# Kernel tuning notes

Hardware: AMD Instinct MI355X
Metric: run time of the kernel (lower is better)

## Reference

```python
import jax, jax.numpy as jnp
import numpy as np

B, S = 2, 2048          # batch, seq_len (tokens flattened to T=B*S)
HID = 2048              # hidden_size
H = 16                  # num_heads
DN, DR, DV = 128, 64, 128   # qk_nope_head_dim, qk_rope_head_dim, v_head_dim
QKD = DN + DR           # qk_head_dim = 192
QLR, KVR = 1536, 512    # q_lora_rank, kv_lora_rank
THETA = 10000.0
EPS = 1e-6
SCALE = QKD ** -0.5


def rmsnorm(x, w):
    return x * jax.lax.rsqrt(jnp.mean(x * x, axis=-1, keepdims=True) + EPS) * w


def rope_gptj(x, pos):
    # non-neox (interleaved / GPT-J) style on partial head dim DR
    # x: [T, Hx, DR], pos: [T]
    half = DR // 2
    inv_freq = 1.0 / (THETA ** (jnp.arange(half, dtype=jnp.float32) * 2.0 / DR))
    ang = pos.astype(jnp.float32)[:, None] * inv_freq[None, :]      # [T, half]
    cos = jnp.cos(ang)[:, None, :]
    sin = jnp.sin(ang)[:, None, :]
    x1 = x[..., 0::2]
    x2 = x[..., 1::2]
    o1 = x1 * cos - x2 * sin
    o2 = x2 * cos + x1 * sin
    return jnp.stack([o1, o2], axis=-1).reshape(x.shape)


def setup_inputs() -> dict:
    key = jax.random.key(0)
    ks = jax.random.split(key, 8)
    T = B * S
    positions = jnp.tile(jnp.arange(S, dtype=jnp.int64 if jax.config.jax_enable_x64 else jnp.int32), B)
    hidden_states = jax.random.normal(ks[0], (T, HID), dtype=jnp.float32)
    s = 0.02
    Wqa = jax.random.normal(ks[1], (HID, QLR), dtype=jnp.float32) * s
    q_a_ln_w = jnp.ones((QLR,), dtype=jnp.float32)
    Wqb = jax.random.normal(ks[2], (QLR, H * QKD), dtype=jnp.float32) * s
    Wkva = jax.random.normal(ks[3], (HID, KVR + DR), dtype=jnp.float32) * s
    kv_a_ln_w = jnp.ones((KVR,), dtype=jnp.float32)
    Wkvb = jax.random.normal(ks[4], (KVR, H * (DN + DV)), dtype=jnp.float32) * s
    Wo = jax.random.normal(ks[5], (H * DV, HID), dtype=jnp.float32) * s
    return {"positions": positions, "hidden_states": hidden_states, "Wqa": Wqa,
            "q_a_ln_w": q_a_ln_w, "Wqb": Wqb, "Wkva": Wkva,
            "kv_a_ln_w": kv_a_ln_w, "Wkvb": Wkvb, "Wo": Wo}


def reference(positions, hidden_states, Wqa, q_a_ln_w, Wqb, Wkva, kv_a_ln_w, Wkvb, Wo):
    T = hidden_states.shape[0]
    # --- Q path: low-rank compression ---
    ckq = hidden_states @ Wqa                       # [T, QLR]
    q_c = rmsnorm(ckq, q_a_ln_w)
    q = (q_c @ Wqb).reshape(T, H, QKD)              # [T, H, 192]
    q_nope, q_pe = q[..., :DN], q[..., DN:]
    # --- KV path: latent compression + shared rope key ---
    kv_no_split = hidden_states @ Wkva              # [T, KVR+DR]
    kv_c, k_pe = kv_no_split[:, :KVR], kv_no_split[:, KVR:]
    kv_c_normed = rmsnorm(kv_c, kv_a_ln_w)
    kv = (kv_c_normed @ Wkvb).reshape(T, H, DN + DV)
    k_nope, v = kv[..., :DN], kv[..., DN:]
    # --- RoPE on partial dims (non-neox) ---
    q_pe = rope_gptj(q_pe, positions)               # [T, H, DR]
    k_pe = rope_gptj(k_pe[:, None, :], positions)   # [T, 1, DR]
    # --- assemble full q/k per batch ---
    qf = jnp.concatenate([q_nope, q_pe], axis=-1).reshape(B, S, H, QKD)
    kf = jnp.concatenate([k_nope, jnp.broadcast_to(k_pe, (T, H, DR))], axis=-1).reshape(B, S, H, QKD)
    vf = v.reshape(B, S, H, DV)
    # --- causal attention ---
    scores = jnp.einsum('bqhd,bkhd->bhqk', qf, kf) * SCALE
    mask = jnp.tril(jnp.ones((S, S), dtype=bool))
    scores = jnp.where(mask[None, None], scores, jnp.finfo(scores.dtype).min)
    probs = jax.nn.softmax(scores, axis=-1)
    attn = jnp.einsum('bhqk,bkhd->bqhd', probs, vf).reshape(T, H * DV)
    # --- output projection ---
    return attn @ Wo                                # [T, HID]
```

## Files before the change

### kernel.cpp

```cpp
#include <hip/hip_runtime.h>
#include <hip/hip_bf16.h>

typedef __hip_bfloat16 bf16;
typedef short bf16x8 __attribute__((ext_vector_type(8)));
typedef float f32x4 __attribute__((ext_vector_type(4)));

#define MFMA16(a, b, c) __builtin_amdgcn_mfma_f32_16x16x32_bf16((a), (b), (c), 0, 0, 0)

__device__ __forceinline__ short f2bs(float f) {
  bf16 h = __float2bfloat16(f);
  return __builtin_bit_cast(short, h);
}
__device__ __forceinline__ float bs2f(short s) {
  return __bfloat162float(__builtin_bit_cast(bf16, s));
}

__device__ __forceinline__ void gload16(const void* g, const void* l) {
  __builtin_amdgcn_global_load_lds(
      (const __attribute__((address_space(1))) unsigned int*)g,
      (__attribute__((address_space(3))) unsigned int*)l, 16, 0, 0);
}

__global__ __launch_bounds__(256) void cvt3(
    const float* __restrict__ s0, bf16* __restrict__ d0, int n0,
    const float* __restrict__ s1, bf16* __restrict__ d1, int n1,
    const float* __restrict__ s2, bf16* __restrict__ d2)
{
  int i = blockIdx.x * 256 + threadIdx.x;
  const float* s; bf16* d; int idx;
  if (i < n0)            { s = s0; d = d0; idx = i; }
  else if (i < n0 + n1)  { s = s1; d = d1; idx = i - n0; }
  else                   { s = s2; d = d2; idx = i - n0 - n1; }
  const float4* sp = (const float4*)s;
  float4 a = sp[2 * idx], b = sp[2 * idx + 1];
  union { uint4 v; short sh[8]; } o;
  o.sh[0] = f2bs(a.x); o.sh[1] = f2bs(a.y); o.sh[2] = f2bs(a.z); o.sh[3] = f2bs(a.w);
  o.sh[4] = f2bs(b.x); o.sh[5] = f2bs(b.y); o.sh[6] = f2bs(b.z); o.sh[7] = f2bs(b.w);
  ((uint4*)d)[idx] = o.v;
}

__global__ __launch_bounds__(256) void t_cvt(const float* __restrict__ src,
                                             bf16* __restrict__ dst, int K, int N) {
  __shared__ __align__(16) short Ts[64][72];
  const long n0 = (long)blockIdx.x * 64, k0 = (long)blockIdx.y * 64;
  const int r = threadIdx.x >> 2, c4 = threadIdx.x & 3;
  const float* s = src + (k0 + r) * (long)N + n0 + c4 * 16;
  #pragma unroll
  for (int j = 0; j < 4; ++j) {
    float4 v = *(const float4*)(s + j * 4);
    Ts[r][c4 * 16 + j * 4 + 0] = f2bs(v.x);
    Ts[r][c4 * 16 + j * 4 + 1] = f2bs(v.y);
    Ts[r][c4 * 16 + j * 4 + 2] = f2bs(v.z);
    Ts[r][c4 * 16 + j * 4 + 3] = f2bs(v.w);
  }
  __syncthreads();
  union { uint4 v; short sh[8]; } o0, o1;
  #pragma unroll
  for (int j = 0; j < 8; ++j) o0.sh[j] = Ts[c4 * 16 + j][r];
  #pragma unroll
  for (int j = 0; j < 8; ++j) o1.sh[j] = Ts[c4 * 16 + 8 + j][r];
  *(uint4*)(dst + (n0 + r) * (long)K + k0 + c4 * 16)     = o0.v;
  *(uint4*)(dst + (n0 + r) * (long)K + k0 + c4 * 16 + 8) = o1.v;
}

template<bool F32OUT>
__device__ __forceinline__ void gemm_core(
    short* As, short* Bs,
    const bf16* __restrict__ A, const bf16* __restrict__ BT, void* __restrict__ Cv,
    int N, int K, int lda, int ldb, int ldc, bf16* __restrict__ C2, int ncut,
    int nx, int nwg, int lin)
{
  const int tid = threadIdx.x, lane = tid & 63, w = tid >> 6;
  const int l15 = lane & 15, l4 = lane >> 4;
  const int wr = w >> 1, wc = w & 1;
  const int sl = (lin & 7) * (nwg >> 3) + (lin >> 3);
  const long bm = (long)(sl / nx) * 128, bn = (long)(sl % nx) * 128;
  f32x4 acc[4][4] = {};

  const int srow = tid >> 3;
  const int scs = (tid & 7) ^ (srow & 7);
  const int rsw = l15 & 7;

  for (int k0 = 0; k0 < K; k0 += 64) {
    __syncthreads();
    #pragma unroll
    for (int j = 0; j < 4; ++j) {
      const unsigned lb = __builtin_amdgcn_readfirstlane((j * 256 + w * 64) * 16);
      gload16(A + (bm + j * 32 + srow) * (long)lda + k0 + scs * 8, (char*)As + lb);
      gload16(BT + (bn + j * 32 + srow) * (long)ldb + k0 + scs * 8, (char*)Bs + lb);
    }
    __syncthreads();
    #pragma unroll
    for (int kk = 0; kk < 2; ++kk) {
      bf16x8 a[4], b[4];
      const int slot = (kk * 4 + l4) ^ rsw;
      #pragma unroll
      for (int mi = 0; mi < 4; ++mi)
        a[mi] = *(const bf16x8*)&As[(wr * 64 + mi * 16 + l15) * 64 + slot * 8];
      #pragma unroll
      for (int ni = 0; ni < 4; ++ni)
        b[ni] = *(const bf16x8*)&Bs[(wc * 64 + ni * 16 + l15) * 64 + slot * 8];
      #pragma unroll
      for (int mi = 0; mi < 4; ++mi)
        #pragma unroll
        for (int ni = 0; ni < 4; ++ni)
          acc[mi][ni] = MFMA16(a[mi], b[ni], acc[mi][ni]);
    }
  }
  #pragma unroll
  for (int mi = 0; mi < 4; ++mi)
    #pragma unroll
    for (int ni = 0; ni < 4; ++ni)
      #pragma unroll
      for (int r = 0; r < 4; ++r) {
        long row = bm + wr * 64 + mi * 16 + l4 * 4 + r;
        long col = bn + wc * 64 + ni * 16 + l15;
        float v = acc[mi][ni][r];
        if (F32OUT) {
          ((float*)Cv)[row * ldc + col] = v;
        } else if (C2 && col >= ncut) {
          C2[row * 640 + (col - ncut)] = __float2bfloat16(v);
        } else {
          ((bf16*)Cv)[row * (long)ldc + col] = __float2bfloat16(v);
        }
      }
}

template<bool F32OUT>
__global__ __launch_bounds__(256) void gemm_v4(
    const bf16* __restrict__ A, const bf16* __restrict__ BT, void* __restrict__ Cv,
    int N, int K, int lda, int ldb, int ldc, bf16* __restrict__ C2, int ncut)
{
  __shared__ __align__(16) short As[128 * 64];
  __shared__ __align__(16) short Bs[128 * 64];
  const int nx = gridDim.x, nwg = nx * gridDim.y;
  const int lin = blockIdx.y * nx + blockIdx.x;
  gemm_core<F32OUT>(As, Bs, A, BT, Cv, N, K, lda, ldb, ldc, C2, ncut, nx, nwg, lin);
}

__global__ __launch_bounds__(256) void gemm_dual(
    const bf16* __restrict__ A0, const bf16* __restrict__ B0, bf16* __restrict__ C0,
    const bf16* __restrict__ A1, const bf16* __restrict__ B1, bf16* __restrict__ C1)
{
  __shared__ __align__(16) short As[128 * 64];
  __shared__ __align__(16) short Bs[128 * 64];
  const int bid = blockIdx.x;
  if (bid < 768)
    gemm_core<false>(As, Bs, A0, B0, C0, 3072, 1536, 1536, 1536, 3072, nullptr, 0,
                     24, 768, bid);
  else
    gemm_core<false>(As, Bs, A1, B1, C1, 4096, 512, 640, 512, 4096, nullptr, 0,
                     32, 1024, bid - 768);
}

template<int C>
__device__ __forceinline__ void rms_core(bf16* __restrict__ xr,
                                         const bf16* __restrict__ w, float* red)
{
  constexpr int PER = C / 256;
  const int tid = threadIdx.x;
  float v[PER];
  float ss = 0.f;
  #pragma unroll
  for (int k = 0; k < PER; ++k) {
    float f = __bfloat162float(xr[tid + k * 256]);
    v[k] = f; ss += f * f;
  }
  #pragma unroll
  for (int off = 1; off < 64; off <<= 1) ss += __shfl_xor(ss, off);
  if ((tid & 63) == 0) red[tid >> 6] = ss;
  __syncthreads();
  float tot = red[0] + red[1] + red[2] + red[3];
  float scale = rsqrtf(tot / (float)C + 1e-6f);
  #pragma unroll
  for (int k = 0; k < PER; ++k)
    xr[tid + k * 256] =
        __float2bfloat16(v[k] * scale * __bfloat162float(w[tid + k * 256]));
}

__global__ __launch_bounds__(256) void rms_dual(bf16* __restrict__ ckq,
                                                const bf16* __restrict__ qw,
                                                bf16* __restrict__ kvns,
                                                const bf16* __restrict__ kvw)
{
  __shared__ float red[4];
  const int bid = blockIdx.x;
  if (bid < 4096) rms_core<1536>(ckq + (long)bid * 1536, qw, red);
  else            rms_core<512>(kvns + (long)(bid - 4096) * 640, kvw, red);
}

__global__ __launch_bounds__(256) void prep_kf(const bf16* __restrict__ kv,
                                               const bf16* __restrict__ kvns,
                                               bf16* __restrict__ Kf)
{
  __shared__ short pe[64];
  const int t = blockIdx.x, tid = threadIdx.x;
  if (tid < 32) {
    int i = tid;
    float p = (float)(t & 2047);
    float freq = powf(10000.0f, -(float)i / 32.0f);
    float sn, cs;
    sincosf(p * freq, &sn, &cs);
    float y1 = __bfloat162float(kvns[(long)t * 640 + 512 + 2 * i]);
    float y2 = __bfloat162float(kvns[(long)t * 640 + 512 + 2 * i + 1]);
    pe[2 * i]     = f2bs(y1 * cs - y2 * sn);
    pe[2 * i + 1] = f2bs(y2 * cs + y1 * sn);
  }
  __syncthreads();
  const int b = t >> 11, ts = t & 2047;
  const int swz = t & 7;
  #pragma unroll
  for (int uu = 0; uu < 2; ++uu) {
    int u = uu * 256 + tid;
    if (u >= 384) break;
    int h = u / 24, s = u % 24;
    int cs = s ^ swz;
    uint4 val;
    if (cs < 16) val = *(const uint4*)(kv + (long)t * 4096 + h * 256 + cs * 8);
    else         val = *(const uint4*)&pe[(cs - 16) * 8];
    *(uint4*)(Kf + ((long)(b * 16 + h) * 2048 + ts) * 192 + s * 8) = val;
  }
}

__global__ __launch_bounds__(256) void prep_vt(const bf16* __restrict__ kv,
                                               bf16* __restrict__ Vt)
{
  __shared__ __align__(16) short Ts[64][136];
  const int kb = blockIdx.x, bh = blockIdx.y, b = bh >> 4, h = bh & 15;
  const int k0 = kb * 64, tid = threadIdx.x;
  #pragma unroll
  for (int j = 0; j < 4; ++j) {
    int u = j * 256 + tid;
    int kr = u >> 4, seg = u & 15;
    *(uint4*)&Ts[kr][seg * 8] = *(const uint4*)(kv +
        (long)(b * 2048 + k0 + kr) * 4096 + h * 256 + 128 + seg * 8);
  }
  __syncthreads();
  #pragma unroll
  for (int j = 0; j < 4; ++j) {
    int u = j * 256 + tid;
    int d = u >> 3, s = u & 7;
    int cs = s ^ (d & 7);
    union { uint4 v; short sh[8]; } o;
    #pragma unroll
    for (int jj = 0; jj < 8; ++jj) o.sh[jj] = Ts[cs * 8 + jj][d];
    *(uint4*)(Vt + ((long)bh * 128 + d) * 2048 + k0 + s * 8) = o.v;
  }
}

__global__ __launch_bounds__(256) void attn_v6(const bf16* __restrict__ q,
                                               const bf16* __restrict__ Kf,
                                               const bf16* __restrict__ Vt,
                                               bf16* __restrict__ attn)
{
  __shared__ __align__(16) short Ks[64 * 192];
  __shared__ __align__(16) short Vs[128 * 64];
  __shared__ __align__(16) short Ps[4][16 * 64];
  const float SC2 = 0.10411442245076847f;
  const int tid = threadIdx.x, lane = tid & 63, w = tid >> 6;
  const int l15 = lane & 15, l4 = lane >> 4;
  const int lin = blockIdx.x;
  const int x = lin & 7, j = lin >> 3;
  const int bh = x * 4 + (j >> 4), p = j & 15;
  const int b = bh >> 4, h = bh & 15;
  const unsigned lbase = __builtin_amdgcn_readfirstlane(w * 64 * 16);

  #pragma unroll
  for (int half = 0; half < 2; ++half) {
    const int qt = half ? (31 - p) : p;
    const long qrow0 = (long)b * 2048 + qt * 64;
    const int rowt = qt * 64 + w * 16 + l15;

    bf16x8 qf[6];
    {
      const short* qrow = (const short*)q + (qrow0 + w * 16 + l15) * 3072 + h * 192;
      #pragma unroll
      for (int kc = 0; kc < 6; ++kc)
        qf[kc] = *(const bf16x8*)(qrow + kc * 32 + l4 * 8);
    }
    {
      float pos = (float)rowt;
      #pragma unroll
      for (int kc = 4; kc < 6; ++kc)
        #pragma unroll
        for (int pr = 0; pr < 4; ++pr) {
          int i = (kc - 4) * 16 + l4 * 4 + pr;
          float freq = __expf((float)i * -0.28782313662425572f);
          float sn, cs;
          sincosf(pos * freq, &sn, &cs);
          float x1 = bs2f(qf[kc][2 * pr]), x2 = bs2f(qf[kc][2 * pr + 1]);
          qf[kc][2 * pr]     = f2bs(x1 * cs - x2 * sn);
          qf[kc][2 * pr + 1] = f2bs(x2 * cs + x1 * sn);
        }
    }
    f32x4 o[8] = {};
    float mreg = -1e30f, ls = 0.f;
    const int nch = qt + 1;

    {
      const char* ksrc = (const char*)(Kf + (long)bh * 2048 * 192);
      #pragma unroll
      for (int jj = 0; jj < 6; ++jj)
        gload16(ksrc + (jj * 256 + tid) * 16, (char*)Ks + jj * 4096 + lbase);
    }
    __syncthreads();

    for (int c = 0; c < nch; ++c) {
      const int k0 = c * 64;
      {
        #pragma unroll
        for (int jj = 0; jj < 4; ++jj) {
          int seg = jj * 256 + tid;
          const bf16* vsrc = Vt + ((long)bh * 128 + (seg >> 3)) * 2048 + k0 + (seg & 7) * 8;
          gload16(vsrc, (char*)Vs + jj * 4096 + lbase);
        }
      }
      __builtin_amdgcn_s_setprio(1);
      f32x4 s[4] = {};
      #pragma unroll
      for (int kc = 0; kc < 6; ++kc)
        #pragma unroll
        for (int kg = 0; kg < 4; ++kg) {
          int row = kg * 16 + l15;
          int slot = (kc * 4 + l4) ^ (l15 & 7);
          bf16x8 kb = *(const bf16x8*)&Ks[row * 192 + slot * 8];
          s[kg] = MFMA16(kb, qf[kc], s[kg]);
        }
      __builtin_amdgcn_s_setprio(0);

      const bool diag = (c == qt);
      float pk[16];
      #pragma unroll
      for (int kg = 0; kg < 4; ++kg)
        #pragma unroll
        for (int r = 0; r < 4; ++r) {
          float v = s[kg][r];
          if (diag && (k0 + kg * 16 + l4 * 4 + r > rowt)) v = -1e30f;
          pk[kg * 4 + r] = v;
        }
      float cm = pk[0];
      #pragma unroll
      for (int i = 1; i < 16; ++i) cm = fmaxf(cm, pk[i]);
      cm = fmaxf(cm, __shfl_xor(cm, 16));
      cm = fmaxf(cm, __shfl_xor(cm, 32));
      cm *= SC2;
      if (__ballot(cm > mreg + 12.0f)) {
        float mn = fmaxf(mreg, cm);
        float al = exp2f(mreg - mn);
        ls *= al;
        float af[4];
        #pragma unroll
        for (int r = 0; r < 4; ++r) af[r] = __shfl(al, l4 * 4 + r);
        #pragma unroll
        for (int f = 0; f < 8; ++f)
          #pragma unroll
          for (int r = 0; r < 4; ++r) o[f][r] *= af[r];
        mreg = mn;
      }
      float ps = 0.f;
      #pragma unroll
      for (int i = 0; i < 16; ++i) {
        pk[i] = exp2f(fmaf(pk[i], SC2, -mreg));
        ps += pk[i];
      }
      ps += __shfl_xor(ps, 16);
      ps += __shfl_xor(ps, 32);
      ls += ps;
      #pragma unroll
      for (int kg = 0; kg < 4; ++kg)
        #pragma unroll
        for (int pr = 0; pr < 2; ++pr) {
          int key2 = kg * 16 + l4 * 4 + pr * 2;
          int sl = (key2 >> 3) ^ (l15 & 7);
          unsigned lo = (unsigned short)f2bs(pk[kg * 4 + pr * 2]);
          unsigned hi = (unsigned short)f2bs(pk[kg * 4 + pr * 2 + 1]);
          *(unsigned*)&Ps[w][l15 * 64 + sl * 8 + (key2 & 7)] = lo | (hi << 16);
        }
      __syncthreads();

      if (c + 1 < nch) {
        const char* ksrc = (const char*)(Kf + ((long)bh * 2048 + k0 + 64) * 192);
        #pragma unroll
        for (int jj = 0; jj < 6; ++jj)
          gload16(ksrc + (jj * 256 + tid) * 16, (char*)Ks + jj * 4096 + lbase);
      }

      __builtin_amdgcn_s_setprio(1);
      #pragma unroll
      for (int ks = 0; ks < 2; ++ks) {
        int psl = (ks * 4 + l4) ^ (l15 & 7);
        bf16x8 pa = *(const bf16x8*)&Ps[w][l15 * 64 + psl * 8];
        #pragma unroll
        for (int f = 0; f < 8; ++f) {
          int vrow = f * 16 + l15;
          int vsl = (ks * 4 + l4) ^ (l15 & 7);
          bf16x8 bv = *(const bf16x8*)&Vs[vrow * 64 + vsl * 8];
          o[f] = MFMA16(pa, bv, o[f]);
        }
      }
      __builtin_amdgcn_s_setprio(0);
      __syncthreads();
    }

    #pragma unroll
    for (int r = 0; r < 4; ++r) {
      float lsr = __shfl(ls, l4 * 4 + r);
      float inv = 1.0f / lsr;
      long t = qrow0 + w * 16 + l4 * 4 + r;
      bf16* dst = attn + t * 2048 + h * 128;
      #pragma unroll
      for (int f = 0; f < 8; ++f)
        dst[f * 16 + l15] = __float2bfloat16(o[f][r] * inv);
    }
  }
}

extern "C" void kernel_launch(void* const* d_in, const int* in_sizes, int n_in,
                              void* d_out, int out_size, void* d_ws, size_t ws_size,
                              hipStream_t stream) {
  const int T = 4096;
  const float* hs_f   = (const float*)d_in[1];
  const float* Wqa_f  = (const float*)d_in[2];
  const float* qln_f  = (const float*)d_in[3];
  const float* Wqb_f  = (const float*)d_in[4];
  const float* Wkva_f = (const float*)d_in[5];
  const float* kvln_f = (const float*)d_in[6];
  const float* Wkvb_f = (const float*)d_in[7];
  const float* Wo_f   = (const float*)d_in[8];

  bf16* base = (bf16*)d_ws;
  bf16* hs_c  = base;
  bf16* ckq   = base + 8388608;
  bf16* qln_c = base + 14680064;
  bf16* kvln_c= base + 14681600;
  bf16* arena = base + 14682112;
  bf16* q     = base + 21497856;
  bf16* kvns  = base + 34080768;
  bf16* kv    = base + 36702208;
  bf16* Vt    = base + 53479424;
  bf16* Kf    = base;
  bf16* attnb = kv;

  cvt3<<<4097, 256, 0, stream>>>(hs_f, hs_c, 1048576, qln_f, qln_c, 192, kvln_f, kvln_c);

  t_cvt<<<dim3(24, 32), 256, 0, stream>>>(Wqa_f, arena, 2048, 1536);
  t_cvt<<<dim3(9, 32), 256, 0, stream>>>(Wkva_f, arena + (size_t)1536 * 2048, 2048, 576);
  gemm_v4<false><<<dim3(17, 32), 256, 0, stream>>>(hs_c, arena, ckq, 2176, 2048,
                                                   2048, 2048, 1536, kvns, 1536);
  rms_dual<<<8192, 256, 0, stream>>>(ckq, qln_c, kvns, kvln_c);
  t_cvt<<<dim3(48, 24), 256, 0, stream>>>(Wqb_f, arena, 1536, 3072);
  t_cvt<<<dim3(64, 8), 256, 0, stream>>>(Wkvb_f, arena + 4718592, 512, 4096);
  gemm_dual<<<1792, 256, 0, stream>>>(ckq, arena, q, kvns, arena + 4718592, kv);
  prep_kf<<<T, 256, 0, stream>>>(kv, kvns, Kf);
  prep_vt<<<dim3(32, 32), 256, 0, stream>>>(kv, Vt);
  attn_v6<<<512, 256, 0, stream>>>(q, Kf, Vt, attnb);
  t_cvt<<<dim3(32, 32), 256, 0, stream>>>(Wo_f, arena, 2048, 2048);
  gemm_v4<true><<<dim3(16, 32), 256, 0, stream>>>(attnb, arena, d_out, 2048, 2048,
                                                  2048, 2048, 2048, nullptr, 0);
}
```

Baseline: 302.2 us.

## Fuse KV-b GEMM epilogue into Kf/Vt layouts and merge conversion kernels

The KV up-projection GEMM now writes its output straight into the swizzled Kf layout (nope half) and, through an LDS transpose, into the Vt layout. This removes the intermediate kv buffer and the separate prep_kf/prep_vt passes. The rope part of Kf is written by a slimmer prep_pe kernel. All weight and activation fp32-to-bf16 conversions are merged into two multi-role launches (prep1, prep2), cutting launch count. The cost is scattered 2-byte stores for the Kf epilogue and a larger LDS footprint in gemm_dual.

```diff
diff --git a/kernel.cpp b/kernel.cpp
--- a/kernel.cpp
+++ b/kernel.cpp
@@ -21,28 +21,10 @@
       (__attribute__((address_space(3))) unsigned int*)l, 16, 0, 0);
 }
 
-__global__ __launch_bounds__(256) void cvt3(
-    const float* __restrict__ s0, bf16* __restrict__ d0, int n0,
-    const float* __restrict__ s1, bf16* __restrict__ d1, int n1,
-    const float* __restrict__ s2, bf16* __restrict__ d2)
-{
-  int i = blockIdx.x * 256 + threadIdx.x;
-  const float* s; bf16* d; int idx;
-  if (i < n0)            { s = s0; d = d0; idx = i; }
-  else if (i < n0 + n1)  { s = s1; d = d1; idx = i - n0; }
-  else                   { s = s2; d = d2; idx = i - n0 - n1; }
-  const float4* sp = (const float4*)s;
-  float4 a = sp[2 * idx], b = sp[2 * idx + 1];
-  union { uint4 v; short sh[8]; } o;
-  o.sh[0] = f2bs(a.x); o.sh[1] = f2bs(a.y); o.sh[2] = f2bs(a.z); o.sh[3] = f2bs(a.w);
-  o.sh[4] = f2bs(b.x); o.sh[5] = f2bs(b.y); o.sh[6] = f2bs(b.z); o.sh[7] = f2bs(b.w);
-  ((uint4*)d)[idx] = o.v;
-}
-
-__global__ __launch_bounds__(256) void t_cvt(const float* __restrict__ src,
-                                             bf16* __restrict__ dst, int K, int N) {
-  __shared__ __align__(16) short Ts[64][72];
-  const long n0 = (long)blockIdx.x * 64, k0 = (long)blockIdx.y * 64;
+__device__ __forceinline__ void t_cvt_core(const float* __restrict__ src,
+                                           bf16* __restrict__ dst, int K, int N,
+                                           int bx, int by, short Ts[64][72]) {
+  const long n0 = (long)bx * 64, k0 = (long)by * 64;
   const int r = threadIdx.x >> 2, c4 = threadIdx.x & 3;
   const float* s = src + (k0 + r) * (long)N + n0 + c4 * 16;
   #pragma unroll
@@ -61,6 +43,48 @@
   for (int j = 0; j < 8; ++j) o1.sh[j] = Ts[c4 * 16 + 8 + j][r];
   *(uint4*)(dst + (n0 + r) * (long)K + k0 + c4 * 16)     = o0.v;
   *(uint4*)(dst + (n0 + r) * (long)K + k0 + c4 * 16 + 8) = o1.v;
+}
+
+__global__ __launch_bounds__(256) void prep1(
+    const float* __restrict__ hs_f, bf16* __restrict__ hs_c,
+    const float* __restrict__ qln_f, bf16* __restrict__ qln_c,
+    const float* __restrict__ kvln_f, bf16* __restrict__ kvln_c,
+    const float* __restrict__ Wqa_f, const float* __restrict__ Wkva_f,
+    bf16* __restrict__ arena)
+{
+  __shared__ __align__(16) short Ts[64][72];
+  const int bid = blockIdx.x;
+  if (bid < 4097) {
+    int i = bid * 256 + threadIdx.x;
+    const float* s; bf16* d; int idx;
+    if (i < 1048576)            { s = hs_f;   d = hs_c;   idx = i; }
+    else if (i < 1048576 + 192) { s = qln_f;  d = qln_c;  idx = i - 1048576; }
+    else                        { s = kvln_f; d = kvln_c; idx = i - 1048768; }
+    const float4* sp = (const float4*)s;
+    float4 a = sp[2 * idx], b = sp[2 * idx + 1];
+    union { uint4 v; short sh[8]; } o;
+    o.sh[0] = f2bs(a.x); o.sh[1] = f2bs(a.y); o.sh[2] = f2bs(a.z); o.sh[3] = f2bs(a.w);
+    o.sh[4] = f2bs(b.x); o.sh[5] = f2bs(b.y); o.sh[6] = f2bs(b.z); o.sh[7] = f2bs(b.w);
+    ((uint4*)d)[idx] = o.v;
+  } else if (bid < 4097 + 768) {
+    int l = bid - 4097;
+    t_cvt_core(Wqa_f, arena, 2048, 1536, l % 24, l / 24, Ts);
+  } else {
+    int l = bid - 4865;
+    t_cvt_core(Wkva_f, arena + (size_t)1536 * 2048, 2048, 576, l % 9, l / 9, Ts);
+  }
+}
+
+__global__ __launch_bounds__(256) void prep2(
+    const float* __restrict__ Wqb_f, bf16* __restrict__ wqbT,
+    const float* __restrict__ Wkvb_f, bf16* __restrict__ wkvbT,
+    const float* __restrict__ Wo_f, bf16* __restrict__ woT)
+{
+  __shared__ __align__(16) short Ts[64][72];
+  const int bid = blockIdx.x;
+  if (bid < 1152)      t_cvt_core(Wqb_f, wqbT, 1536, 3072, bid % 48, bid / 48, Ts);
+  else if (bid < 1664) { int l = bid - 1152; t_cvt_core(Wkvb_f, wkvbT, 512, 4096, l % 64, l / 64, Ts); }
+  else                 { int l = bid - 1664; t_cvt_core(Wo_f, woT, 2048, 2048, l % 32, l / 32, Ts); }
 }
 
 template<bool F32OUT>
@@ -139,18 +163,100 @@
 }
 
 __global__ __launch_bounds__(256) void gemm_dual(
-    const bf16* __restrict__ A0, const bf16* __restrict__ B0, bf16* __restrict__ C0,
-    const bf16* __restrict__ A1, const bf16* __restrict__ B1, bf16* __restrict__ C1)
-{
-  __shared__ __align__(16) short As[128 * 64];
-  __shared__ __align__(16) short Bs[128 * 64];
+    const bf16* __restrict__ ckq, const bf16* __restrict__ wqbT, bf16* __restrict__ q,
+    const bf16* __restrict__ kvns, const bf16* __restrict__ wkvbT,
+    bf16* __restrict__ Kf, bf16* __restrict__ Vt)
+{
+  __shared__ __align__(16) short LDSU[17408];
+  short* As = LDSU;
+  short* Bs = LDSU + 8192;
   const int bid = blockIdx.x;
-  if (bid < 768)
-    gemm_core<false>(As, Bs, A0, B0, C0, 3072, 1536, 1536, 1536, 3072, nullptr, 0,
+  if (bid < 768) {
+    gemm_core<false>(As, Bs, ckq, wqbT, q, 3072, 1536, 1536, 1536, 3072, nullptr, 0,
                      24, 768, bid);
-  else
-    gemm_core<false>(As, Bs, A1, B1, C1, 4096, 512, 640, 512, 4096, nullptr, 0,
-                     32, 1024, bid - 768);
+    return;
+  }
+  const int lin = bid - 768;
+  const int tid = threadIdx.x, lane = tid & 63, w = tid >> 6;
+  const int l15 = lane & 15, l4 = lane >> 4;
+  const int wr = w >> 1, wc = w & 1;
+  const int sl = (lin & 7) * 128 + (lin >> 3);
+  const long bm = (long)(sl / 32) * 128, bn = (long)(sl % 32) * 128;
+  f32x4 acc[4][4] = {};
+  const int srow = tid >> 3;
+  const int scs = (tid & 7) ^ (srow & 7);
+  const int rsw = l15 & 7;
+
+  for (int k0 = 0; k0 < 512; k0 += 64) {
+    __syncthreads();
+    #pragma unroll
+    for (int j = 0; j < 4; ++j) {
+      const unsigned lb = __builtin_amdgcn_readfirstlane((j * 256 + w * 64) * 16);
+      gload16(kvns + (bm + j * 32 + srow) * 640L + k0 + scs * 8, (char*)As + lb);
+      gload16(wkvbT + (bn + j * 32 + srow) * 512L + k0 + scs * 8, (char*)Bs + lb);
+    }
+    __syncthreads();
+    #pragma unroll
+    for (int kk = 0; kk < 2; ++kk) {
+      bf16x8 a[4], b[4];
+      const int slot = (kk * 4 + l4) ^ rsw;
+      #pragma unroll
+      for (int mi = 0; mi < 4; ++mi)
+        a[mi] = *(const bf16x8*)&As[(wr * 64 + mi * 16 + l15) * 64 + slot * 8];
+      #pragma unroll
+      for (int ni = 0; ni < 4; ++ni)
+        b[ni] = *(const bf16x8*)&Bs[(wc * 64 + ni * 16 + l15) * 64 + slot * 8];
+      #pragma unroll
+      for (int mi = 0; mi < 4; ++mi)
+        #pragma unroll
+        for (int ni = 0; ni < 4; ++ni)
+          acc[mi][ni] = MFMA16(a[mi], b[ni], acc[mi][ni]);
+    }
+  }
+
+  const int h = (int)(bn >> 8);
+  const int lc = (int)(bn & 255);
+  const int bh = (int)(bm >> 11) * 16 + h;
+
+  if (lc == 0) {
+    #pragma unroll
+    for (int mi = 0; mi < 4; ++mi)
+      #pragma unroll
+      for (int ni = 0; ni < 4; ++ni) {
+        const int col = wc * 64 + ni * 16 + l15;
+        const int cs = col >> 3, e = col & 7;
+        #pragma unroll
+        for (int r = 0; r < 4; ++r) {
+          int t = (int)bm + wr * 64 + mi * 16 + l4 * 4 + r;
+          Kf[((size_t)bh * 2048 + (t & 2047)) * 192 + ((cs ^ (t & 7)) << 3) + e] =
+              __float2bfloat16(acc[mi][ni][r]);
+        }
+      }
+  } else {
+    __syncthreads();
+    #pragma unroll
+    for (int mi = 0; mi < 4; ++mi)
+      #pragma unroll
+      for (int ni = 0; ni < 4; ++ni)
+        #pragma unroll
+        for (int r = 0; r < 4; ++r)
+          LDSU[(wr * 64 + mi * 16 + l4 * 4 + r) * 136 + wc * 64 + ni * 16 + l15] =
+              f2bs(acc[mi][ni][r]);
+    __syncthreads();
+    #pragma unroll
+    for (int j = 0; j < 8; ++j) {
+      int u = j * 256 + tid;
+      int d = u >> 4, slo = u & 15;
+      int k0l = (slo >> 3) << 6;
+      int cs = slo & 7;
+      int tb = k0l + cs * 8;
+      union { uint4 v; short sh[8]; } o;
+      #pragma unroll
+      for (int i = 0; i < 8; ++i) o.sh[i] = LDSU[(tb + i) * 136 + d];
+      *(uint4*)(Vt + ((size_t)(bh * 128 + d)) * 2048 + (int)(bm & 2047) + k0l +
+                ((cs ^ (d & 7)) << 3)) = o.v;
+    }
+  }
 }
 
 template<int C>
@@ -189,8 +295,7 @@
   else            rms_core<512>(kvns + (long)(bid - 4096) * 640, kvw, red);
 }
 
-__global__ __launch_bounds__(256) void prep_kf(const bf16* __restrict__ kv,
-                                               const bf16* __restrict__ kvns,
+__global__ __launch_bounds__(256) void prep_pe(const bf16* __restrict__ kvns,
                                                bf16* __restrict__ Kf)
 {
   __shared__ short pe[64];
@@ -207,44 +312,12 @@
     pe[2 * i + 1] = f2bs(y2 * cs + y1 * sn);
   }
   __syncthreads();
-  const int b = t >> 11, ts = t & 2047;
-  const int swz = t & 7;
-  #pragma unroll
-  for (int uu = 0; uu < 2; ++uu) {
-    int u = uu * 256 + tid;
-    if (u >= 384) break;
-    int h = u / 24, s = u % 24;
-    int cs = s ^ swz;
-    uint4 val;
-    if (cs < 16) val = *(const uint4*)(kv + (long)t * 4096 + h * 256 + cs * 8);
-    else         val = *(const uint4*)&pe[(cs - 16) * 8];
-    *(uint4*)(Kf + ((long)(b * 16 + h) * 2048 + ts) * 192 + s * 8) = val;
-  }
-}
-
-__global__ __launch_bounds__(256) void prep_vt(const bf16* __restrict__ kv,
-                                               bf16* __restrict__ Vt)
-{
-  __shared__ __align__(16) short Ts[64][136];
-  const int kb = blockIdx.x, bh = blockIdx.y, b = bh >> 4, h = bh & 15;
-  const int k0 = kb * 64, tid = threadIdx.x;
-  #pragma unroll
-  for (int j = 0; j < 4; ++j) {
-    int u = j * 256 + tid;
-    int kr = u >> 4, seg = u & 15;
-    *(uint4*)&Ts[kr][seg * 8] = *(const uint4*)(kv +
-        (long)(b * 2048 + k0 + kr) * 4096 + h * 256 + 128 + seg * 8);
-  }
-  __syncthreads();
-  #pragma unroll
-  for (int j = 0; j < 4; ++j) {
-    int u = j * 256 + tid;
-    int d = u >> 3, s = u & 7;
-    int cs = s ^ (d & 7);
-    union { uint4 v; short sh[8]; } o;
-    #pragma unroll
-    for (int jj = 0; jj < 8; ++jj) o.sh[jj] = Ts[cs * 8 + jj][d];
-    *(uint4*)(Vt + ((long)bh * 128 + d) * 2048 + k0 + s * 8) = o.v;
+  if (tid < 128) {
+    const int hh = tid >> 3, j = tid & 7;
+    const int swz = t & 7;
+    const int b = t >> 11, ts = t & 2047;
+    uint4 val = *(const uint4*)&pe[(j ^ swz) * 8];
+    *(uint4*)(Kf + ((size_t)(b * 16 + hh) * 2048 + ts) * 192 + (16 + j) * 8) = val;
   }
 }
 
@@ -430,31 +503,26 @@
 
   bf16* base = (bf16*)d_ws;
   bf16* hs_c  = base;
+  bf16* woT   = base;
   bf16* ckq   = base + 8388608;
   bf16* qln_c = base + 14680064;
   bf16* kvln_c= base + 14681600;
   bf16* arena = base + 14682112;
   bf16* q     = base + 21497856;
   bf16* kvns  = base + 34080768;
-  bf16* kv    = base + 36702208;
-  bf16* Vt    = base + 53479424;
-  bf16* Kf    = base;
-  bf16* attnb = kv;
-
-  cvt3<<<4097, 256, 0, stream>>>(hs_f, hs_c, 1048576, qln_f, qln_c, 192, kvln_f, kvln_c);
-
-  t_cvt<<<dim3(24, 32), 256, 0, stream>>>(Wqa_f, arena, 2048, 1536);
-  t_cvt<<<dim3(9, 32), 256, 0, stream>>>(Wkva_f, arena + (size_t)1536 * 2048, 2048, 576);
+  bf16* Kf    = base + 36702208;
+  bf16* Vt    = base + 49285120;
+  bf16* attnb = ckq;
+
+  prep1<<<5153, 256, 0, stream>>>(hs_f, hs_c, qln_f, qln_c, kvln_f, kvln_c,
+                                  Wqa_f, Wkva_f, arena);
   gemm_v4<false><<<dim3(17, 32), 256, 0, stream>>>(hs_c, arena, ckq, 2176, 2048,
                                                    2048, 2048, 1536, kvns, 1536);
   rms_dual<<<8192, 256, 0, stream>>>(ckq, qln_c, kvns, kvln_c);
-  t_cvt<<<dim3(48, 24), 256, 0, stream>>>(Wqb_f, arena, 1536, 3072);
-  t_cvt<<<dim3(64, 8), 256, 0, stream>>>(Wkvb_f, arena + 4718592, 512, 4096);
-  gemm_dual<<<1792, 256, 0, stream>>>(ckq, arena, q, kvns, arena + 4718592, kv);
-  prep_kf<<<T, 256, 0, stream>>>(kv, kvns, Kf);
-  prep_vt<<<dim3(32, 32), 256, 0, stream>>>(kv, Vt);
+  prep_pe<<<T, 256, 0, stream>>>(kvns, Kf);
+  prep2<<<2688, 256, 0, stream>>>(Wqb_f, arena, Wkvb_f, arena + 4718592, Wo_f, woT);
+  gemm_dual<<<1792, 256, 0, stream>>>(ckq, arena, q, kvns, arena + 4718592, Kf, Vt);
   attn_v6<<<512, 256, 0, stream>>>(q, Kf, Vt, attnb);
-  t_cvt<<<dim3(32, 32), 256, 0, stream>>>(Wo_f, arena, 2048, 2048);
-  gemm_v4<true><<<dim3(16, 32), 256, 0, stream>>>(attnb, arena, d_out, 2048, 2048,
+  gemm_v4<true><<<dim3(16, 32), 256, 0, stream>>>(attnb, woT, d_out, 2048, 2048,
                                                   2048, 2048, 2048, nullptr, 0);
 }
```

Result: faster. 293.6 us (-2.9%).
